# Kernel tuning notes

Measured on AMD Instinct MI355X. Metric: run time of the kernel, lower is better.

The kernel has to match this reference:

```python
import jax, jax.numpy as jnp
import numpy as np

B, T, D, H, C, M = 32, 64, 300, 256, 5, 64  # batch, seq, word_dim, rnn_size, classes, n_mention_masks


def _lstm_dir(x, length, W, b, reverse):
    """TF1 LSTMCell (gate order i, j, f, o; forget_bias=1.0) with sequence_length
    semantics of tf.nn.bidirectional_rnn: outputs past length are zero, state is
    copied through. x: [B, T, Din] -> outputs [B, T, H]."""
    Bx, Tx, Din = x.shape
    Hh = b.shape[0] // 4
    xs = jnp.moveaxis(x, 1, 0)                      # [T, B, Din]
    ts = jnp.arange(Tx)
    if reverse:
        xs = xs[::-1]
        ts = Tx - 1 - ts                             # original time index after flip

    def step(carry, inp):
        h, c = carry
        xt, t = inp
        z = jnp.concatenate([xt, h], axis=-1) @ W + b    # [B, 4H]
        i, j, f, o = jnp.split(z, 4, axis=-1)
        c_new = jax.nn.sigmoid(f + 1.0) * c + jax.nn.sigmoid(i) * jnp.tanh(j)
        h_new = jax.nn.sigmoid(o) * jnp.tanh(c_new)
        m = (t < length)[:, None]
        h_out = jnp.where(m, h_new, 0.0)
        return (jnp.where(m, h_new, h), jnp.where(m, c_new, c)), h_out

    init = (jnp.zeros((Bx, Hh), x.dtype), jnp.zeros((Bx, Hh), x.dtype))
    _, outs = jax.lax.scan(step, init, (xs, ts))     # [T, B, H]
    if reverse:
        outs = outs[::-1]
    return jnp.moveaxis(outs, 0, 1)                  # [B, T, H]


def setup_inputs() -> dict:
    key = jax.random.key(0)
    ks = jax.random.split(key, 10)
    def xavier(k, shape):
        fan_in = shape[0]
        return (jax.random.normal(k, shape, jnp.float32) / np.sqrt(fan_in)).astype(jnp.float32)
    return {
        "input_data": jax.random.normal(ks[0], (B, T, D), jnp.float32),
        "entMentIndex": jax.random.uniform(ks[1], (M, B, T, 2 * H), jnp.float32),
        "output_data": jax.random.randint(ks[2], (M // T, T, C), 0, 2, jnp.int32),
        "W_fw": xavier(ks[3], (D + H, 4 * H)),
        "b_fw": jnp.zeros((4 * H,), jnp.float32),
        "W_bw": xavier(ks[4], (D + H, 4 * H)),
        "b_bw": jnp.zeros((4 * H,), jnp.float32),
        "W1": xavier(ks[5], (2 * H, H)),
        "b1": jnp.full((H,), 0.1, jnp.float32),
        "W2": xavier(ks[6], (H, C)),
        "b2": jnp.full((C,), 0.1, jnp.float32),
    }


def reference(input_data, entMentIndex, output_data, W_fw, b_fw, W_bw, b_bw, W1, b1, W2, b2):
    # sequence lengths from non-zero timesteps (all == T for randn inputs)
    used = jnp.sign(jnp.max(jnp.abs(input_data), axis=2))
    length = jnp.sum(used, axis=1).astype(jnp.int32)            # [B]

    out_f = _lstm_dir(input_data, length, W_fw, b_fw, reverse=False)
    out_b = _lstm_dir(input_data, length, W_bw, b_bw, reverse=True)
    output = jnp.concatenate([out_f, out_b], axis=-1)           # [B, T, 2H]

    # tf.scan's lambda ignores the accumulator -> features[m] = output * entMentIndex[m]
    # output_f = mean_T( sum_B( features ) )  ==  einsum / T
    output_f = jnp.einsum('mbtd,btd->md', entMentIndex, output) / T  # [M, 2H]

    l1 = jax.nn.relu(output_f @ W1 + b1)                         # [M, H]
    pred = jax.nn.sigmoid(l1 @ W2 + b2)                          # [M, C]
    prediction = pred.reshape(-1, T, C)                          # [M//T, T, C]

    labels = output_data.astype(prediction.dtype)
    ce = -jnp.sum(labels * jnp.log(prediction), axis=1)          # sum over time
    loss = jnp.mean(ce)
    return prediction, loss
```

## Files before the change

### kernel.cpp

```cpp
#include <hip/hip_runtime.h>
#include <math.h>

#define B_   32
#define T_   64
#define D_   300
#define H_   256
#define G4H  1024
#define M_   64
#define C_   5

typedef _Float16 h2v __attribute__((ext_vector_type(2)));
typedef _Float16 h8  __attribute__((ext_vector_type(8)));
typedef float    f4  __attribute__((ext_vector_type(4)));

__device__ __forceinline__ float sigmoidf_(float x) { return 1.0f / (1.0f + expf(-x)); }

__device__ __forceinline__ float dot2_(h2v a, h2v b, float c) {
#if __has_builtin(__builtin_amdgcn_fdot2)
    return __builtin_amdgcn_fdot2(a, b, c, false);
#else
    return c + (float)a[0] * (float)b[0] + (float)a[1] * (float)b[1];
#endif
}

__global__ void __launch_bounds__(1024)
k_length(const float* __restrict__ x, int* __restrict__ length) {
    const int b   = blockIdx.x;
    const int tid = threadIdx.x;
    const int t   = tid >> 4;
    const int j   = tid & 15;

    __shared__ int cnt;
    if (tid == 0) cnt = 0;
    __syncthreads();

    const float* row = x + (size_t)(b * T_ + t) * D_;
    float mv = 0.f;
    #pragma unroll
    for (int i = 0; i < 19; ++i) {
        int d = j + 16 * i;
        if (d < D_) mv = fmaxf(mv, fabsf(row[d]));
    }
    #pragma unroll
    for (int off = 8; off >= 1; off >>= 1) mv = fmaxf(mv, __shfl_xor(mv, off));
    if (j == 0 && mv > 0.f) atomicAdd(&cnt, 1);
    __syncthreads();
    if (tid == 0) length[b] = cnt;
}

__global__ void __launch_bounds__(256)
k_xw(const float* __restrict__ x,
     const float* __restrict__ Wfw, const float* __restrict__ bfw,
     const float* __restrict__ Wbw, const float* __restrict__ bbw,
     float* __restrict__ xw) {
    const int nt  = blockIdx.x;
    const int mt  = blockIdx.y;
    const int tid = threadIdx.x;
    const int w   = tid >> 6;
    const int l   = tid & 63;
    const int n0  = nt * 128, m0 = mt * 128;
    const int dir = n0 >> 10;
    const float* W    = dir ? Wbw : Wfw;
    const float* bias = dir ? bbw : bfw;
    const int ncol0 = n0 & 1023;

    __shared__ __align__(16) _Float16 As[128][40];
    __shared__ __align__(16) _Float16 Bs[128][40];

    f4 acc[4][4];
    #pragma unroll
    for (int i = 0; i < 4; ++i)
        #pragma unroll
        for (int j = 0; j < 4; ++j) acc[i][j] = (f4){0.f, 0.f, 0.f, 0.f};

    const int wr = (w >> 1) * 64;
    const int wc = (w & 1) * 64;

    for (int k0 = 0; k0 < 320; k0 += 32) {
        #pragma unroll
        for (int p = 0; p < 4; ++p) {
            int row = (tid >> 3) + p * 32;
            int kq  = tid & 7;
            int k   = k0 + kq * 4;
            f4 v = (k < D_) ? *(const f4*)&x[(size_t)(m0 + row) * D_ + k]
                            : (f4){0.f, 0.f, 0.f, 0.f};
            _Float16* dst = &As[row][kq * 4];
            dst[0] = (_Float16)v[0]; dst[1] = (_Float16)v[1];
            dst[2] = (_Float16)v[2]; dst[3] = (_Float16)v[3];
        }
        #pragma unroll
        for (int p = 0; p < 4; ++p) {
            int kk   = (tid >> 5) + p * 8;
            int colq = tid & 31;
            int k    = k0 + kk;
            f4 v = (k < D_) ? *(const f4*)&W[(size_t)k * G4H + ncol0 + colq * 4]
                            : (f4){0.f, 0.f, 0.f, 0.f};
            #pragma unroll
            for (int i = 0; i < 4; ++i) Bs[colq * 4 + i][kk] = (_Float16)v[i];
        }
        __syncthreads();

        h8 afr[4], bfr[4];
        #pragma unroll
        for (int fr = 0; fr < 4; ++fr)
            afr[fr] = *(const h8*)&As[wr + fr * 16 + (l & 15)][(l >> 4) * 8];
        #pragma unroll
        for (int fc = 0; fc < 4; ++fc)
            bfr[fc] = *(const h8*)&Bs[wc + fc * 16 + (l & 15)][(l >> 4) * 8];
        #pragma unroll
        for (int fr = 0; fr < 4; ++fr)
            #pragma unroll
            for (int fc = 0; fc < 4; ++fc)
                acc[fr][fc] = __builtin_amdgcn_mfma_f32_16x16x32_f16(
                    afr[fr], bfr[fc], acc[fr][fc], 0, 0, 0);
        __syncthreads();
    }

    #pragma unroll
    for (int fc = 0; fc < 4; ++fc) {
        int col = ncol0 + wc + fc * 16 + (l & 15);
        float bv = bias[col];
        #pragma unroll
        for (int fr = 0; fr < 4; ++fr) {
            #pragma unroll
            for (int e = 0; e < 4; ++e) {
                int row = m0 + wr + fr * 16 + (l >> 4) * 4 + e;
                xw[(size_t)dir * 2048 * G4H + (size_t)row * G4H + col] =
                    acc[fr][fc][e] + bv;
            }
        }
    }
}

__global__ void __launch_bounds__(512)
k_lstm(const float* __restrict__ Wfw, const float* __restrict__ Wbw,
       const float* __restrict__ xw, const int* __restrict__ length,
       const float* __restrict__ ent, float* __restrict__ partials,
       unsigned* __restrict__ exbuf) {
    const int bid = blockIdx.x;
    const int js  = bid >> 6;
    const int g   = bid & 63;
    const int dir = g >> 5;
    const int b   = g & 31;
    const int tid = threadIdx.x;
    const int w   = tid >> 6;
    const int l   = tid & 63;
    const int c     = w * 32 + (l & 31);
    const int khalf = l >> 5;
    const int colg  = (c >> 6) * 256 + js * 64 + (c & 63);
    const int m8  = tid >> 3;
    const int oct = tid & 7;

    __shared__ __align__(8) _Float16 hl_h[256];
    __shared__ float zfin[256];
    __shared__ float ho_l[64];

    const float* Wg = dir ? Wbw : Wfw;

    h2v wreg[64];
    #pragma unroll
    for (int p = 0; p < 64; ++p) {
        int k = khalf * 128 + 2 * p;
        float w0 = Wg[(size_t)(D_ + k) * G4H + colg];
        float w1 = Wg[(size_t)(D_ + k + 1) * G4H + colg];
        h2v t; t[0] = (_Float16)w0; t[1] = (_Float16)w1;
        wreg[p] = t;
    }

    if (tid < 256) hl_h[tid] = (_Float16)0.f;
    const int len = length[b];
    const size_t xrow = (size_t)(dir * B_ + b) * T_;
    const float* entp = ent + (((size_t)m8 * B_ + b) * T_) * 512
                            + dir * 256 + js * 64 + oct * 8;
    f4 accA = (f4){0.f, 0.f, 0.f, 0.f};
    f4 accB = (f4){0.f, 0.f, 0.f, 0.f};
    __syncthreads();

    float cst = 0.f, hprev = 0.f;

    for (int s = 0; s < T_; ++s) {
        const int tt = dir ? (T_ - 1 - s) : s;
        const unsigned tag = ((unsigned)(s >> 2) & 1u) ^ 1u;
        const size_t slotBase = ((size_t)g * 4 + (s & 3)) * 256;

        f4 e0 = __builtin_nontemporal_load((const f4*)(entp + (size_t)tt * 512));
        f4 e1 = __builtin_nontemporal_load((const f4*)(entp + (size_t)tt * 512 + 4));

        float xv = 0.f;
        if (l < 32) xv = __builtin_nontemporal_load(&xw[(xrow + tt) * G4H + colg]);

        float acc = 0.f;
        const uint2* hp = (const uint2*)&hl_h[khalf * 128];
        #pragma unroll
        for (int j = 0; j < 32; ++j) {
            uint2 hv = hp[j];
            acc = dot2_(wreg[2 * j],     __builtin_bit_cast(h2v, hv.x), acc);
            acc = dot2_(wreg[2 * j + 1], __builtin_bit_cast(h2v, hv.y), acc);
        }
        acc += __shfl_xor(acc, 32);
        if (l < 32) zfin[c] = acc + xv;
        __syncthreads();

        if (tid < 64) {
            float zi = zfin[tid], zj = zfin[64 + tid], zf = zfin[128 + tid], zo = zfin[192 + tid];
            float cn = sigmoidf_(zf + 1.0f) * cst + sigmoidf_(zi) * tanhf(zj);
            float hn = sigmoidf_(zo) * tanhf(cn);
            bool  msk = (tt < len);
            float ho  = msk ? hn : 0.f;
            float hk2 = msk ? hn : hprev;
            if (msk) cst = cn;
            hprev = hk2;
            int jglob = js * 64 + tid;
            ho_l[tid] = ho;
            hl_h[jglob] = (_Float16)hk2;
            unsigned bits = (__float_as_uint(hk2) & ~1u) | tag;
            __hip_atomic_store(&exbuf[slotBase + jglob], bits,
                               __ATOMIC_RELAXED, __HIP_MEMORY_SCOPE_AGENT);
        }

        if (tid < 256 && (tid >> 6) != js) {
            unsigned v; unsigned it = 0;
            for (;;) {
                v = __hip_atomic_load(&exbuf[slotBase + tid],
                                      __ATOMIC_RELAXED, __HIP_MEMORY_SCOPE_AGENT);
                if ((v & 1u) == tag) break;
                __builtin_amdgcn_s_sleep(1);
                if (++it > (1u << 20)) break;
            }
            hl_h[tid] = (_Float16)__uint_as_float(v);
        }
        __syncthreads();

        #pragma unroll
        for (int i = 0; i < 4; ++i) {
            accA[i] += e0[i] * ho_l[oct * 8 + i];
            accB[i] += e1[i] * ho_l[oct * 8 + 4 + i];
        }
    }

    float* pp = partials + ((size_t)m8 * B_ + b) * 512 + dir * 256 + js * 64 + oct * 8;
    *(f4*)pp = accA;
    *(f4*)(pp + 4) = accB;
}

__global__ void k_l1(const float* __restrict__ partials, const float* __restrict__ W1,
                     const float* __restrict__ b1, float* __restrict__ l1) {
    const int m = blockIdx.x;
    const int j = threadIdx.x;
    __shared__ float of[512];
    for (int d = j; d < 512; d += 256) {
        float s = 0.f;
        #pragma unroll
        for (int cc = 0; cc < 32; ++cc) s += partials[((size_t)m * B_ + cc) * 512 + d];
        of[d] = s * (1.0f / T_);
    }
    __syncthreads();
    float z = b1[j];
    for (int k = 0; k < 512; ++k) z += of[k] * W1[(size_t)k * H_ + j];
    l1[(size_t)m * H_ + j] = fmaxf(z, 0.f);
}

__global__ void k_head(const float* __restrict__ l1, const float* __restrict__ W2,
                       const float* __restrict__ b2, const int* __restrict__ labels,
                       float* __restrict__ out) {
    const int tid = threadIdx.x;
    __shared__ float red[320];
    float term = 0.f;
    if (tid < 320) {
        int m = tid / 5, cc = tid % 5;
        float z = b2[cc];
        for (int k = 0; k < H_; ++k) z += l1[(size_t)m * H_ + k] * W2[(size_t)k * C_ + cc];
        float p = 1.f / (1.f + expf(-z));
        out[tid] = p;
        term = -(float)labels[tid] * logf(p);
    }
    red[tid] = term;
    __syncthreads();
    if (tid == 0) {
        float s = 0.f;
        for (int i = 0; i < 320; ++i) s += red[i];
        out[320] = s / (float)C_;
    }
}

extern "C" void kernel_launch(void* const* d_in, const int* in_sizes, int n_in,
                              void* d_out, int out_size, void* d_ws, size_t ws_size,
                              hipStream_t stream) {
    const float* x      = (const float*)d_in[0];
    const float* ent    = (const float*)d_in[1];
    const int*   labels = (const int*)d_in[2];
    const float* Wfw    = (const float*)d_in[3];
    const float* bfw    = (const float*)d_in[4];
    const float* Wbw    = (const float*)d_in[5];
    const float* bbw    = (const float*)d_in[6];
    const float* W1     = (const float*)d_in[7];
    const float* b1     = (const float*)d_in[8];
    const float* W2     = (const float*)d_in[9];
    const float* b2     = (const float*)d_in[10];
    float* out = (float*)d_out;

    float*    ws       = (float*)d_ws;
    float*    xw       = ws;
    unsigned* exbuf    = (unsigned*)(xw + 4194304);
    float*    l1       = (float*)(exbuf + 65536);
    int*      length   = (int*)(l1 + 16384);
    float*    partials = (float*)(length + 32);

    k_length<<<32, 1024, 0, stream>>>(x, length);
    k_xw<<<dim3(16, 16), 256, 0, stream>>>(x, Wfw, bfw, Wbw, bbw, xw);
    k_lstm<<<256, 512, 0, stream>>>(Wfw, Wbw, xw, length, ent, partials, exbuf);
    k_l1<<<64, 256, 0, stream>>>(partials, W1, b1, l1);
    k_head<<<1, 320, 0, stream>>>(l1, W2, b2, labels, out);
}
```

Before: 216.5 us.

## Interleave two batch rows per LSTM block to hide cross-block exchange latency

Each LSTM block now processes two independent batch sequences (b and b+16) with the same register-resident weights, halving the grid to 128 blocks. Phases are staggered so the dot product for sequence B runs while sequence A's hidden-state exchange is in flight, and the ent/xw loads switch from nontemporal to normal loads. The aim is to hide the global-memory polling latency of the recurrent exchange behind useful work and to reuse the weight registers. The cost is more barriers per step, twice the serial gate and dot work per block, and fewer blocks filling the GPU.

```diff
diff --git a/kernel.cpp b/kernel.cpp
--- a/kernel.cpp
+++ b/kernel.cpp
@@ -132,16 +132,70 @@
     }
 }
 
-__global__ void __launch_bounds__(512)
+__device__ __forceinline__ void dot_phase(const _Float16* HL, float* ZF,
+                                          const h2v* wreg, float xv,
+                                          int khalf, int c, int l) {
+    float acc = 0.f;
+    const uint2* hp = (const uint2*)(HL + khalf * 128);
+    #pragma unroll
+    for (int j = 0; j < 32; ++j) {
+        uint2 hv = hp[j];
+        acc = dot2_(wreg[2 * j],     __builtin_bit_cast(h2v, hv.x), acc);
+        acc = dot2_(wreg[2 * j + 1], __builtin_bit_cast(h2v, hv.y), acc);
+    }
+    acc += __shfl_xor(acc, 32);
+    if (l < 32) ZF[c] = acc + xv;
+}
+
+__device__ __forceinline__ void gates_phase(const float* ZF, float* HO, _Float16* HL,
+                                            unsigned* exslot, float& cst, float& hprev,
+                                            int len, int tt, unsigned tag,
+                                            int tid, int js) {
+    if (tid < 64) {
+        float zi = ZF[tid], zj = ZF[64 + tid], zf = ZF[128 + tid], zo = ZF[192 + tid];
+        float cn = sigmoidf_(zf + 1.0f) * cst + sigmoidf_(zi) * tanhf(zj);
+        float hn = sigmoidf_(zo) * tanhf(cn);
+        bool  msk = (tt < len);
+        float ho  = msk ? hn : 0.f;
+        float hk2 = msk ? hn : hprev;
+        if (msk) cst = cn;
+        hprev = hk2;
+        HO[tid] = ho;
+        HL[js * 64 + tid] = (_Float16)hk2;
+        unsigned bits = (__float_as_uint(hk2) & ~1u) | tag;
+        __hip_atomic_store(&exslot[js * 64 + tid], bits,
+                           __ATOMIC_RELAXED, __HIP_MEMORY_SCOPE_AGENT);
+    }
+}
+
+__device__ __forceinline__ void poll_phase(_Float16* HL, unsigned* exslot,
+                                           unsigned tag, int tid, int js) {
+    if (tid < 256 && (tid >> 6) != js) {
+        unsigned v; unsigned it = 0;
+        for (;;) {
+            v = __hip_atomic_load(&exslot[tid],
+                                  __ATOMIC_RELAXED, __HIP_MEMORY_SCOPE_AGENT);
+            if ((v & 1u) == tag) break;
+            __builtin_amdgcn_s_sleep(1);
+            if (++it > (1u << 20)) break;
+        }
+        HL[tid] = (_Float16)__uint_as_float(v);
+    }
+}
+
+__global__ void __launch_bounds__(512, 2)
 k_lstm(const float* __restrict__ Wfw, const float* __restrict__ Wbw,
        const float* __restrict__ xw, const int* __restrict__ length,
        const float* __restrict__ ent, float* __restrict__ partials,
        unsigned* __restrict__ exbuf) {
     const int bid = blockIdx.x;
-    const int js  = bid >> 6;
-    const int g   = bid & 63;
-    const int dir = g >> 5;
-    const int b   = g & 31;
+    const int js  = bid >> 5;
+    const int pg  = bid & 31;
+    const int dir = pg >> 4;
+    const int b0  = pg & 15;
+    const int b1  = b0 + 16;
+    const int gA  = dir * 32 + b0;
+    const int gB  = dir * 32 + b1;
     const int tid = threadIdx.x;
     const int w   = tid >> 6;
     const int l   = tid & 63;
@@ -151,9 +205,12 @@
     const int m8  = tid >> 3;
     const int oct = tid & 7;
 
-    __shared__ __align__(8) _Float16 hl_h[256];
-    __shared__ float zfin[256];
-    __shared__ float ho_l[64];
+    __shared__ __align__(8) _Float16 hl_A[256];
+    __shared__ __align__(8) _Float16 hl_B[256];
+    __shared__ float zfin_A[256];
+    __shared__ float zfin_B[256];
+    __shared__ float ho_A[64];
+    __shared__ float ho_B[64];
 
     const float* Wg = dir ? Wbw : Wfw;
 
@@ -167,80 +224,69 @@
         wreg[p] = t;
     }
 
-    if (tid < 256) hl_h[tid] = (_Float16)0.f;
-    const int len = length[b];
-    const size_t xrow = (size_t)(dir * B_ + b) * T_;
-    const float* entp = ent + (((size_t)m8 * B_ + b) * T_) * 512
-                            + dir * 256 + js * 64 + oct * 8;
-    f4 accA = (f4){0.f, 0.f, 0.f, 0.f};
-    f4 accB = (f4){0.f, 0.f, 0.f, 0.f};
-    __syncthreads();
-
-    float cst = 0.f, hprev = 0.f;
+    if (tid < 256) { hl_A[tid] = (_Float16)0.f; hl_B[tid] = (_Float16)0.f; }
+    const int lenA = length[b0];
+    const int lenB = length[b1];
+    const size_t xrowA = (size_t)(dir * B_ + b0) * T_;
+    const size_t xrowB = (size_t)(dir * B_ + b1) * T_;
+    const float* entpA = ent + (((size_t)m8 * B_ + b0) * T_) * 512
+                             + dir * 256 + js * 64 + oct * 8;
+    const float* entpB = ent + (((size_t)m8 * B_ + b1) * T_) * 512
+                             + dir * 256 + js * 64 + oct * 8;
+    f4 aA0 = (f4){0.f, 0.f, 0.f, 0.f}, aA1 = (f4){0.f, 0.f, 0.f, 0.f};
+    f4 aB0 = (f4){0.f, 0.f, 0.f, 0.f}, aB1 = (f4){0.f, 0.f, 0.f, 0.f};
+    __syncthreads();
+
+    float cstA = 0.f, hprevA = 0.f;
+    float cstB = 0.f, hprevB = 0.f;
 
     for (int s = 0; s < T_; ++s) {
         const int tt = dir ? (T_ - 1 - s) : s;
         const unsigned tag = ((unsigned)(s >> 2) & 1u) ^ 1u;
-        const size_t slotBase = ((size_t)g * 4 + (s & 3)) * 256;
-
-        f4 e0 = __builtin_nontemporal_load((const f4*)(entp + (size_t)tt * 512));
-        f4 e1 = __builtin_nontemporal_load((const f4*)(entp + (size_t)tt * 512 + 4));
-
-        float xv = 0.f;
-        if (l < 32) xv = __builtin_nontemporal_load(&xw[(xrow + tt) * G4H + colg]);
-
-        float acc = 0.f;
-        const uint2* hp = (const uint2*)&hl_h[khalf * 128];
-        #pragma unroll
-        for (int j = 0; j < 32; ++j) {
-            uint2 hv = hp[j];
-            acc = dot2_(wreg[2 * j],     __builtin_bit_cast(h2v, hv.x), acc);
-            acc = dot2_(wreg[2 * j + 1], __builtin_bit_cast(h2v, hv.y), acc);
-        }
-        acc += __shfl_xor(acc, 32);
-        if (l < 32) zfin[c] = acc + xv;
-        __syncthreads();
-
-        if (tid < 64) {
-            float zi = zfin[tid], zj = zfin[64 + tid], zf = zfin[128 + tid], zo = zfin[192 + tid];
-            float cn = sigmoidf_(zf + 1.0f) * cst + sigmoidf_(zi) * tanhf(zj);
-            float hn = sigmoidf_(zo) * tanhf(cn);
-            bool  msk = (tt < len);
-            float ho  = msk ? hn : 0.f;
-            float hk2 = msk ? hn : hprev;
-            if (msk) cst = cn;
-            hprev = hk2;
-            int jglob = js * 64 + tid;
-            ho_l[tid] = ho;
-            hl_h[jglob] = (_Float16)hk2;
-            unsigned bits = (__float_as_uint(hk2) & ~1u) | tag;
-            __hip_atomic_store(&exbuf[slotBase + jglob], bits,
-                               __ATOMIC_RELAXED, __HIP_MEMORY_SCOPE_AGENT);
-        }
-
-        if (tid < 256 && (tid >> 6) != js) {
-            unsigned v; unsigned it = 0;
-            for (;;) {
-                v = __hip_atomic_load(&exbuf[slotBase + tid],
-                                      __ATOMIC_RELAXED, __HIP_MEMORY_SCOPE_AGENT);
-                if ((v & 1u) == tag) break;
-                __builtin_amdgcn_s_sleep(1);
-                if (++it > (1u << 20)) break;
-            }
-            hl_h[tid] = (_Float16)__uint_as_float(v);
-        }
-        __syncthreads();
-
+        unsigned* slotA = exbuf + ((size_t)gA * 4 + (s & 3)) * 256;
+        unsigned* slotB = exbuf + ((size_t)gB * 4 + (s & 3)) * 256;
+
+        f4 eA0 = *(const f4*)(entpA + (size_t)tt * 512);
+        f4 eA1 = *(const f4*)(entpA + (size_t)tt * 512 + 4);
+        f4 eB0 = *(const f4*)(entpB + (size_t)tt * 512);
+        f4 eB1 = *(const f4*)(entpB + (size_t)tt * 512 + 4);
+        float xvA = 0.f, xvB = 0.f;
+        if (l < 32) {
+            xvA = xw[(xrowA + tt) * G4H + colg];
+            xvB = xw[(xrowB + tt) * G4H + colg];
+        }
+
+        dot_phase(hl_A, zfin_A, wreg, xvA, khalf, c, l);
+        __syncthreads();
+
+        gates_phase(zfin_A, ho_A, hl_A, slotA, cstA, hprevA, lenA, tt, tag, tid, js);
+        dot_phase(hl_B, zfin_B, wreg, xvB, khalf, c, l);
+        __syncthreads();
+
+        gates_phase(zfin_B, ho_B, hl_B, slotB, cstB, hprevB, lenB, tt, tag, tid, js);
         #pragma unroll
         for (int i = 0; i < 4; ++i) {
-            accA[i] += e0[i] * ho_l[oct * 8 + i];
-            accB[i] += e1[i] * ho_l[oct * 8 + 4 + i];
-        }
-    }
-
-    float* pp = partials + ((size_t)m8 * B_ + b) * 512 + dir * 256 + js * 64 + oct * 8;
-    *(f4*)pp = accA;
-    *(f4*)(pp + 4) = accB;
+            aA0[i] += eA0[i] * ho_A[oct * 8 + i];
+            aA1[i] += eA1[i] * ho_A[oct * 8 + 4 + i];
+        }
+        poll_phase(hl_A, slotA, tag, tid, js);
+        __syncthreads();
+
+        #pragma unroll
+        for (int i = 0; i < 4; ++i) {
+            aB0[i] += eB0[i] * ho_B[oct * 8 + i];
+            aB1[i] += eB1[i] * ho_B[oct * 8 + 4 + i];
+        }
+        poll_phase(hl_B, slotB, tag, tid, js);
+        __syncthreads();
+    }
+
+    float* pA = partials + ((size_t)m8 * B_ + b0) * 512 + dir * 256 + js * 64 + oct * 8;
+    *(f4*)pA = aA0;
+    *(f4*)(pA + 4) = aA1;
+    float* pB = partials + ((size_t)m8 * B_ + b1) * 512 + dir * 256 + js * 64 + oct * 8;
+    *(f4*)pB = aB0;
+    *(f4*)(pB + 4) = aB1;
 }
 
 __global__ void k_l1(const float* __restrict__ partials, const float* __restrict__ W1,
@@ -308,7 +354,7 @@
 
     k_length<<<32, 1024, 0, stream>>>(x, length);
     k_xw<<<dim3(16, 16), 256, 0, stream>>>(x, Wfw, bfw, Wbw, bbw, xw);
-    k_lstm<<<256, 512, 0, stream>>>(Wfw, Wbw, xw, length, ent, partials, exbuf);
+    k_lstm<<<128, 512, 0, stream>>>(Wfw, Wbw, xw, length, ent, partials, exbuf);
     k_l1<<<64, 256, 0, stream>>>(partials, W1, b1, l1);
     k_head<<<1, 320, 0, stream>>>(l1, W2, b2, labels, out);
 }
```

After: 301.8 us. 1.39x slower.
